# Kernel optimization log

Measured on AMD Instinct MI355X. Metric: run time of the kernel, lower is better.

The kernel has to match this reference:

```python
import jax, jax.numpy as jnp
import numpy as np

B, S, D, H = 4, 2048, 1024, 4
HD = D // H


def setup_inputs() -> dict:
    key = jax.random.key(0)
    ks = jax.random.split(key, 6)
    s = 0.02  # init scale for projection weights
    return {
        "hidden_states": jax.random.normal(ks[0], (B, S, D), jnp.float32),
        "Wq": jax.random.normal(ks[1], (D, D), jnp.float32) * s,
        "Wk": jax.random.normal(ks[2], (D, D), jnp.float32) * s,
        "Wv": jax.random.normal(ks[3], (D, D), jnp.float32) * s,
        "Wo": jax.random.normal(ks[4], (D, D), jnp.float32) * s,
        "bo": jnp.zeros((D,), jnp.float32),
        "betas": jax.random.normal(ks[5], (1, H, 1, 1), jnp.float32),
        "mem": jnp.zeros((H, HD, HD), jnp.float32),
        "z": jnp.zeros((H, HD, 1), jnp.float32),
    }


def reference(hidden_states, Wq, Wk, Wv, Wo, bo, betas, mem, z):
    b, s, d = hidden_states.shape
    h = betas.shape[1]
    hd = d // h

    def split(x):  # [b,s,d] -> [b,h,s,hd]
        return x.reshape(b, s, h, hd).transpose(0, 2, 1, 3)

    q = split(hidden_states @ Wq.T)
    k = split(hidden_states @ Wk.T)
    v = split(hidden_states @ Wv.T)

    # standard causal attention (note: no 1/sqrt(d) scaling, faithful to source)
    aw = jnp.einsum('bhqd,bhkd->bhqk', q, k)
    causal = jnp.tril(jnp.ones((s, s), bool))
    aw = jnp.where(causal, aw, jnp.finfo(aw.dtype).min)
    p = jax.nn.softmax(aw, axis=-1)
    attn = jnp.einsum('bhqk,bhkd->bhqd', p, v)

    # linear-attention memory read
    sq = jax.nn.elu(q) + 1.0
    sk = jax.nn.elu(k) + 1.0
    A_mem = jnp.einsum('bhsd,hde->bhse', sq, mem) / (
        jnp.einsum('bhsd,hdo->bhso', sq, z) + 1e-6)

    # sigmoid-gated blend
    g = jax.nn.sigmoid(betas)
    out = g * A_mem + (1.0 - g) * attn

    # memory / z state update (delta rule), averaged over batch
    delta = jnp.einsum('bhsd,hde->bhse', sk, mem) / (
        jnp.einsum('bhsd,hdo->bhso', sk, z) + 1e-6)
    mem_new = mem + jnp.einsum('bhsd,bhse->hde', sk, v - delta) / b
    z_new = z + jnp.mean(jnp.sum(sk, axis=2), axis=0)[:, :, None]

    # merge heads + output projection
    out = out.transpose(0, 2, 1, 3).reshape(b, s, d)
    out = out @ Wo.T + bo
    return (out, mem_new, z_new)
```

## Files before the change

kernel.cpp:

```cpp
#include <hip/hip_runtime.h>

#define Bsz 4
#define Ssz 2048
#define Dsz 1024
#define Hsz 4
#define HDsz 256
#define Msz 8192
#define LOG2E 1.4426950408889634f

typedef unsigned short u16;
typedef __attribute__((ext_vector_type(8))) short bf16x8;
typedef __attribute__((ext_vector_type(4))) float f32x4;

__device__ __forceinline__ u16 f2b(float f) {
  unsigned u = __float_as_uint(f);
  return (u16)((u + 0x7FFFu + ((u >> 16) & 1u)) >> 16);
}
__device__ __forceinline__ unsigned pk2(float a, float b) {
  return (unsigned)f2b(a) | ((unsigned)f2b(b) << 16);
}
__device__ __forceinline__ float ex2(float x) {
#if __has_builtin(__builtin_amdgcn_exp2f)
  return __builtin_amdgcn_exp2f(x);
#else
  return exp2f(x);
#endif
}

typedef const unsigned int __attribute__((address_space(1)))* gcp;
typedef unsigned int __attribute__((address_space(3)))* lcp;
__device__ __forceinline__ void gld16(const u16* g, u16* l) {
  __builtin_amdgcn_global_load_lds((gcp)g, (lcp)l, 16, 0, 0);
}

__global__ __launch_bounds__(256) void cvt_bf16(const float4* __restrict__ in,
                                                u16* __restrict__ outp) {
  size_t i = (size_t)blockIdx.x * 256 + threadIdx.x;
  float4 v = in[i];
  uint2 r; r.x = pk2(v.x, v.y); r.y = pk2(v.z, v.w);
  *(uint2*)(outp + i * 4) = r;
}

__global__ __launch_bounds__(256) void gemm_lds(const u16* __restrict__ A16,
                                                const u16* __restrict__ Wb,
                                                const float* __restrict__ bias,
                                                float* __restrict__ C32,
                                                u16* __restrict__ Cbf,
                                                float cbfs) {
  __shared__ u16 sA[128 * 64];
  __shared__ u16 sB[128 * 64];
  const int tid = threadIdx.x;
  const int lane = tid & 63, quad = lane >> 4, l15 = lane & 15;
  const int w = tid >> 6;
  const int mw = (w >> 1) * 64, nw = (w & 1) * 64;
  const int bid = blockIdx.y * 8 + blockIdx.x;
  const int nb = (bid & 7) * 64 + (bid >> 3);
  const int m0 = (nb >> 3) * 128, n0 = (nb & 7) * 128;
  const int r0 = tid >> 3;
  const int seg = ((tid & 7) ^ (r0 & 7)) * 8;
  const u16* ga0 = A16 + (size_t)(m0 + r0) * Dsz + seg;
  const u16* gb0 = Wb + (size_t)(n0 + r0) * Dsz + seg;
  f32x4 acc[4][4] = {};
  for (int k0 = 0; k0 < Dsz; k0 += 64) {
    __syncthreads();
#pragma unroll
    for (int i = 0; i < 4; ++i) {
      gld16(ga0 + (size_t)(i * 32) * Dsz + k0, sA + i * 2048 + w * 512);
      gld16(gb0 + (size_t)(i * 32) * Dsz + k0, sB + i * 2048 + w * 512);
    }
    __syncthreads();
#pragma unroll
    for (int dd = 0; dd < 2; ++dd) {
      bf16x8 af[4], bfr[4];
#pragma unroll
      for (int i = 0; i < 4; ++i) {
        const int sl = ((quad + 4 * dd) ^ (l15 & 7)) * 8;
        af[i] = *(const bf16x8*)&sA[(mw + i * 16 + l15) * 64 + sl];
        bfr[i] = *(const bf16x8*)&sB[(nw + i * 16 + l15) * 64 + sl];
      }
#pragma unroll
      for (int i = 0; i < 4; ++i)
#pragma unroll
        for (int j = 0; j < 4; ++j)
          acc[i][j] = __builtin_amdgcn_mfma_f32_16x16x32_bf16(af[i], bfr[j], acc[i][j], 0, 0, 0);
    }
  }
#pragma unroll
  for (int j = 0; j < 4; ++j) {
    const int n = n0 + nw + j * 16 + l15;
    const float bv = bias ? bias[n] : 0.f;
#pragma unroll
    for (int i = 0; i < 4; ++i) {
#pragma unroll
      for (int r = 0; r < 4; ++r) {
        const int m = m0 + mw + i * 16 + quad * 4 + r;
        const float val = acc[i][j][r] + bv;
        const size_t idx = (size_t)m * Dsz + n;
        if (C32) C32[idx] = val;
        if (Cbf) Cbf[idx] = f2b(val * cbfs);
      }
    }
  }
}

__global__ __launch_bounds__(256) void transpose_v(const float* __restrict__ V,
                                                   u16* __restrict__ Vt) {
  __shared__ u16 tile[32 * 36];
  const int t = threadIdx.x;
  const int s0 = blockIdx.x * 32, e0 = blockIdx.y * 32, bh = blockIdx.z;
  const int b = bh >> 2, h = bh & 3;
  {
    const int s_l = t >> 3, e8 = (t & 7) * 4;
    float4 v = *(const float4*)(V + ((size_t)(b * Ssz) + s0 + s_l) * Dsz + h * HDsz + e0 + e8);
    uint2 r; r.x = pk2(v.x, v.y); r.y = pk2(v.z, v.w);
    *(uint2*)&tile[s_l * 36 + e8] = r;
  }
  __syncthreads();
  {
    const int e_l = t >> 3, s4 = (t & 7) * 4;
    u16 a = tile[(s4 + 0) * 36 + e_l], b2 = tile[(s4 + 1) * 36 + e_l];
    u16 c = tile[(s4 + 2) * 36 + e_l], d = tile[(s4 + 3) * 36 + e_l];
    uint2 r; r.x = (unsigned)a | ((unsigned)b2 << 16);
    r.y = (unsigned)c | ((unsigned)d << 16);
    *(uint2*)(Vt + ((size_t)bh * HDsz + e0 + e_l) * Ssz + s0 + s4) = r;
  }
}

__global__ __launch_bounds__(256) void attn_mfma(const u16* __restrict__ Qg,
                                                 const u16* __restrict__ Kg,
                                                 const u16* __restrict__ Vtg,
                                                 float* __restrict__ At,
                                                 float* __restrict__ Pb,
                                                 float* __restrict__ mlb) {
  static const unsigned char tab[52] = {
      (unsigned char)(31|0x80), (unsigned char)(31|0xC0),
      (unsigned char)(30|0x80), (unsigned char)(30|0xC0),
      (unsigned char)(29|0x80), (unsigned char)(29|0xC0),
      (unsigned char)(28|0x80), (unsigned char)(28|0xC0),
      (unsigned char)(27|0x80), (unsigned char)(27|0xC0),
      (unsigned char)(26|0x80), (unsigned char)(26|0xC0),
      (unsigned char)(25|0x80), (unsigned char)(25|0xC0),
      (unsigned char)(24|0x80), (unsigned char)(24|0xC0),
      (unsigned char)(23|0x80), (unsigned char)(23|0xC0),
      11,
      (unsigned char)(22|0x80), (unsigned char)(22|0xC0),
      (unsigned char)(21|0x80), (unsigned char)(21|0xC0),
      10,
      (unsigned char)(20|0x80), (unsigned char)(20|0xC0),
      (unsigned char)(19|0x80), (unsigned char)(19|0xC0),
      9,
      (unsigned char)(18|0x80), (unsigned char)(18|0xC0),
      (unsigned char)(17|0x80), (unsigned char)(17|0xC0),
      8,
      (unsigned char)(16|0x80), (unsigned char)(16|0xC0),
      (unsigned char)(15|0x80), (unsigned char)(15|0xC0),
      7,
      (unsigned char)(14|0x80), (unsigned char)(14|0xC0),
      (unsigned char)(13|0x80), (unsigned char)(13|0xC0),
      6,
      (unsigned char)(12|0x80), (unsigned char)(12|0xC0),
      5, 4, 3, 2, 1, 0};
  const int e = tab[blockIdx.x];
  const int qt = e & 63, cc = (e >> 6) & 1;
  const bool split = (e >> 7) != 0;
  const int bh = blockIdx.y, b = bh >> 2, h = bh & 3;
  const int tid = threadIdx.x, w = tid >> 6, lane = tid & 63;
  const int quad = lane >> 4, l15 = lane & 15;
  __shared__ u16 sK[2][32 * 256];
  __shared__ u16 sV[256 * 32];
  const int q0w = qt * 64 + w * 16;
  bf16x8 qf[8];
  {
    const u16* qp = Qg + ((size_t)(b * Ssz) + q0w + l15) * Dsz + h * HDsz + quad * 8;
#pragma unroll
    for (int dd = 0; dd < 8; ++dd) qf[dd] = *(const bf16x8*)(qp + dd * 32);
  }
  f32x4 o[16] = {};
  float m_old = -1e30f, l = 0.f;
  const int nkt = 2 * qt + 2, half = qt + 1;
  const int kt_lo = (split && cc) ? half : 0;
  const int kt_hi = (split && !cc) ? half : nkt;
  const u16* kstage = Kg + ((size_t)(b * Ssz) + (tid >> 5)) * Dsz + h * HDsz
                      + (((tid & 31) ^ ((tid >> 5) & 7)) << 3);
  const u16* vstage = Vtg + ((size_t)bh * HDsz + (tid >> 2)) * Ssz
                      + (((tid & 3) ^ ((tid >> 3) & 3)) << 3);
  int bufc = 0;
  {
    const u16* kp = kstage + (size_t)(kt_lo * 32) * Dsz;
#pragma unroll
    for (int i = 0; i < 4; ++i)
      gld16(kp + (size_t)i * 8 * Dsz, &sK[0][w * 512 + i * 2048]);
  }
  for (int kt = kt_lo; kt < kt_hi; ++kt) {
    const int j0 = kt * 32;
    __syncthreads();
    {
      const u16* vp = vstage + kt * 32;
#pragma unroll
      for (int i = 0; i < 4; ++i)
        gld16(vp + (size_t)i * 64 * Ssz, &sV[w * 512 + i * 2048]);
    }
    if (kt + 1 < kt_hi) {
      const u16* kp = kstage + (size_t)((kt + 1) * 32) * Dsz;
      const int bn = bufc ^ 1;
#pragma unroll
      for (int i = 0; i < 4; ++i)
        gld16(kp + (size_t)i * 8 * Dsz, &sK[bn][w * 512 + i * 2048]);
    }
    f32x4 s0a = {}, s0b = {}, s1a = {}, s1b = {};
#pragma unroll
    for (int dd = 0; dd < 4; ++dd) {
      const int c0 = ((dd * 4 + quad) ^ (l15 & 7)) << 3;
      const int c1 = (((dd + 4) * 4 + quad) ^ (l15 & 7)) << 3;
      bf16x8 a0 = *(const bf16x8*)&sK[bufc][l15 * 256 + c0];
      bf16x8 a1 = *(const bf16x8*)&sK[bufc][(16 + l15) * 256 + c0];
      bf16x8 b0 = *(const bf16x8*)&sK[bufc][l15 * 256 + c1];
      bf16x8 b1 = *(const bf16x8*)&sK[bufc][(16 + l15) * 256 + c1];
      s0a = __builtin_amdgcn_mfma_f32_16x16x32_bf16(a0, qf[dd], s0a, 0, 0, 0);
      s1a = __builtin_amdgcn_mfma_f32_16x16x32_bf16(a1, qf[dd], s1a, 0, 0, 0);
      s0b = __builtin_amdgcn_mfma_f32_16x16x32_bf16(b0, qf[dd + 4], s0b, 0, 0, 0);
      s1b = __builtin_amdgcn_mfma_f32_16x16x32_bf16(b1, qf[dd + 4], s1b, 0, 0, 0);
    }
    f32x4 s0v = s0a + s0b, s1v = s1a + s1b;
    const int qg = q0w + l15;
    float p[8];
#pragma unroll
    for (int r = 0; r < 4; ++r) {
      const int kg = j0 + quad * 4 + r;
      p[r] = (kg <= qg) ? s0v[r] : -1e30f;
      p[4 + r] = (kg + 16 <= qg) ? s1v[r] : -1e30f;
    }
    float mt = fmaxf(fmaxf(fmaxf(p[0], p[1]), fmaxf(p[2], p[3])),
                     fmaxf(fmaxf(p[4], p[5]), fmaxf(p[6], p[7])));
    mt = fmaxf(mt, __shfl_xor(mt, 16));
    mt = fmaxf(mt, __shfl_xor(mt, 32));
    const bool keep = __all(mt - m_old <= 11.0f);
    const float m_new = keep ? m_old : fmaxf(m_old, mt);
    float ts = 0.f;
#pragma unroll
    for (int i = 0; i < 8; ++i) { p[i] = ex2(p[i] - m_new); ts += p[i]; }
    ts += __shfl_xor(ts, 16);
    ts += __shfl_xor(ts, 32);
    if (keep) {
      l += ts;
    } else {
      const float alpha = ex2(m_old - m_new);
      l = l * alpha + ts;
      m_old = m_new;
      const float a0_ = __shfl(alpha, (lane & 48) | (quad * 4 + 0));
      const float a1_ = __shfl(alpha, (lane & 48) | (quad * 4 + 1));
      const float a2_ = __shfl(alpha, (lane & 48) | (quad * 4 + 2));
      const float a3_ = __shfl(alpha, (lane & 48) | (quad * 4 + 3));
#pragma unroll
      for (int ds = 0; ds < 16; ++ds) {
        o[ds][0] *= a0_; o[ds][1] *= a1_; o[ds][2] *= a2_; o[ds][3] *= a3_;
      }
    }
    const unsigned a0p = pk2(p[0], p[1]), a1p = pk2(p[2], p[3]);
    const unsigned b0p = pk2(p[4], p[5]), b1p = pk2(p[6], p[7]);
    const int sAl = l15 | ((quad & 1) << 5);
    const int sBl = sAl | 16;
    const unsigned xa0 = __shfl(a0p, sAl), xa1 = __shfl(a1p, sAl);
    const unsigned xb0 = __shfl(b0p, sAl), xb1 = __shfl(b1p, sAl);
    const unsigned ya0 = __shfl(a0p, sBl), ya1 = __shfl(a1p, sBl);
    const unsigned yb0 = __shfl(b0p, sBl), yb1 = __shfl(b1p, sBl);
    const bool hi2 = quad >= 2;
    uint4 pkv;
    pkv.x = hi2 ? xb0 : xa0;
    pkv.y = hi2 ? xb1 : xa1;
    pkv.z = hi2 ? yb0 : ya0;
    pkv.w = hi2 ? yb1 : ya1;
    bf16x8 pf = *(bf16x8*)&pkv;
    const int vc0 = (quad ^ ((l15 >> 1) & 3)) << 3;
    __syncthreads();
#pragma unroll
    for (int ds = 0; ds < 16; ++ds) {
      bf16x8 bv = *(const bf16x8*)&sV[(ds * 16 + l15) * 32 + vc0];
      o[ds] = __builtin_amdgcn_mfma_f32_16x16x32_bf16(pf, bv, o[ds], 0, 0, 0);
    }
    bufc ^= 1;
  }
  if (!split) {
    float lr[4];
#pragma unroll
    for (int r = 0; r < 4; ++r) lr[r] = 1.f / __shfl(l, (lane & 48) | (quad * 4 + r));
    float* ob = At + ((size_t)bh * Ssz + q0w + quad * 4) * HDsz + l15;
#pragma unroll
    for (int r = 0; r < 4; ++r)
#pragma unroll
      for (int ds = 0; ds < 16; ++ds)
        ob[(size_t)r * HDsz + ds * 16] = o[ds][r] * lr[r];
  } else {
    float* dst;
    if (cc == 0)
      dst = At + ((size_t)bh * Ssz + q0w + quad * 4) * HDsz + l15;
    else
      dst = Pb + ((size_t)((bh * 20 + (qt - 12)) * 64) + w * 16 + quad * 4) * HDsz + l15;
#pragma unroll
    for (int r = 0; r < 4; ++r)
#pragma unroll
      for (int ds = 0; ds < 16; ++ds)
        dst[(size_t)r * HDsz + ds * 16] = o[ds][r];
    if (lane < 16) {
      const int idx = (bh * 20 + (qt - 12)) * 64 + w * 16 + l15;
      mlb[cc * 40960 + idx] = m_old;
      mlb[cc * 40960 + 20480 + idx] = l;
    }
  }
}

__global__ __launch_bounds__(256) void attn_merge(float* __restrict__ At,
                                                  const float* __restrict__ Pb,
                                                  const float* __restrict__ mlb) {
  const int qx = blockIdx.x, bh = blockIdx.y;
  const int t = threadIdx.x;
  const int slot = (bh * 20 + qx) * 64;
  float4* abase = (float4*)(At + ((size_t)bh * Ssz + (12 + qx) * 64) * HDsz);
  const float4* pbase = (const float4*)(Pb + (size_t)slot * HDsz);
#pragma unroll
  for (int i = 0; i < 16; ++i) {
    const int f = i * 256 + t;
    const int qr = f >> 6;
    const int idx = slot + qr;
    const float m0 = mlb[idx], l0 = mlb[20480 + idx];
    const float m1 = mlb[40960 + idx], l1 = mlb[61440 + idx];
    const float mm = fmaxf(m0, m1);
    const float w0 = ex2(m0 - mm), w1 = ex2(m1 - mm);
    const float inv = 1.f / (l0 * w0 + l1 * w1);
    float4 av = abase[f];
    float4 pv = pbase[f];
    float4 ov;
    ov.x = (av.x * w0 + pv.x * w1) * inv;
    ov.y = (av.y * w0 + pv.y * w1) * inv;
    ov.z = (av.z * w0 + pv.z * w1) * inv;
    ov.w = (av.w * w0 + pv.w * w1) * inv;
    abase[f] = ov;
  }
}

__global__ __launch_bounds__(256) void eludens(float* __restrict__ Qb,
                                               float* __restrict__ Kb,
                                               const float* __restrict__ z,
                                               float* __restrict__ dq,
                                               float* __restrict__ dk) {
  const int wid = threadIdx.x >> 6, lane = threadIdx.x & 63;
  const int r = blockIdx.x * 4 + wid;
  const int b = r >> 13, h = (r >> 11) & 3, s = r & 2047;
  const size_t base = ((size_t)(b * Ssz + s)) * Dsz + h * HDsz + lane * 4;
  float4 z4 = *(const float4*)(z + h * HDsz + lane * 4);
  float4 q = *(float4*)(Qb + base);
  q.x = q.x > 0.f ? q.x + 1.f : __expf(q.x);
  q.y = q.y > 0.f ? q.y + 1.f : __expf(q.y);
  q.z = q.z > 0.f ? q.z + 1.f : __expf(q.z);
  q.w = q.w > 0.f ? q.w + 1.f : __expf(q.w);
  *(float4*)(Qb + base) = q;
  float4 k = *(float4*)(Kb + base);
  k.x = k.x > 0.f ? k.x + 1.f : __expf(k.x);
  k.y = k.y > 0.f ? k.y + 1.f : __expf(k.y);
  k.z = k.z > 0.f ? k.z + 1.f : __expf(k.z);
  k.w = k.w > 0.f ? k.w + 1.f : __expf(k.w);
  *(float4*)(Kb + base) = k;
  float pq = q.x * z4.x + q.y * z4.y + q.z * z4.z + q.w * z4.w;
  float pk = k.x * z4.x + k.y * z4.y + k.z * z4.z + k.w * z4.w;
#pragma unroll
  for (int off = 32; off; off >>= 1) {
    pq += __shfl_down(pq, off);
    pk += __shfl_down(pk, off);
  }
  if (lane == 0) { dq[r] = pq; dk[r] = pk; }
}

__global__ __launch_bounds__(256) void memread_mfma(const float* __restrict__ Asrc,
                                                    const float* __restrict__ mem,
                                                    const float* __restrict__ dens,
                                                    const float* __restrict__ betas,
                                                    const float* __restrict__ At,
                                                    float* __restrict__ Vio,
                                                    u16* __restrict__ bfout, int mode) {
  const int h = blockIdx.z;
  const int tid = threadIdx.x, lane = tid & 63, w = tid >> 6;
  const int quad = lane >> 4, l15 = lane & 15;
  const int mw = (w >> 1) * 64, ew = (w & 1) * 64;
  const int m0 = blockIdx.y * 128, e0t = blockIdx.x * 128;
  __shared__ u16 sA[128 * 40];
  __shared__ u16 sB[128 * 40];
  const int srow = tid >> 1, sseg = (tid & 1) * 16;
  const int k4 = (tid & 7) * 4, e4 = (tid >> 3) * 4;
  f32x4 acc[4][4] = {};
  for (int k0 = 0; k0 < HDsz; k0 += 32) {
    __syncthreads();
    {
      const float* ap = Asrc + (size_t)(m0 + srow) * Dsz + h * HDsz + k0 + sseg;
      float4 f0 = *(const float4*)ap, f1 = *(const float4*)(ap + 4);
      float4 f2 = *(const float4*)(ap + 8), f3 = *(const float4*)(ap + 12);
      uint4 u0, u1;
      u0.x = pk2(f0.x, f0.y); u0.y = pk2(f0.z, f0.w);
      u0.z = pk2(f1.x, f1.y); u0.w = pk2(f1.z, f1.w);
      u1.x = pk2(f2.x, f2.y); u1.y = pk2(f2.z, f2.w);
      u1.z = pk2(f3.x, f3.y); u1.w = pk2(f3.z, f3.w);
      u16* dst = &sA[srow * 40 + sseg];
      *(uint4*)dst = u0; *(uint4*)(dst + 8) = u1;
    }
    {
      const float* bp = mem + (size_t)h * 65536 + (size_t)(k0 + k4) * HDsz + e0t + e4;
      float4 r0 = *(const float4*)bp;
      float4 r1 = *(const float4*)(bp + HDsz);
      float4 r2 = *(const float4*)(bp + 2 * HDsz);
      float4 r3 = *(const float4*)(bp + 3 * HDsz);
      const float* rr[4] = {(const float*)&r0, (const float*)&r1,
                            (const float*)&r2, (const float*)&r3};
#pragma unroll
      for (int c = 0; c < 4; ++c) {
        uint2 u;
        u.x = pk2(rr[0][c], rr[1][c]);
        u.y = pk2(rr[2][c], rr[3][c]);
        *(uint2*)&sB[(e4 + c) * 40 + k4] = u;
      }
    }
    __syncthreads();
    bf16x8 af[4], bfr[4];
#pragma unroll
    for (int i = 0; i < 4; ++i) {
      af[i] = *(const bf16x8*)&sA[(mw + i * 16 + l15) * 40 + quad * 8];
      bfr[i] = *(const bf16x8*)&sB[(ew + i * 16 + l15) * 40 + quad * 8];
    }
#pragma unroll
    for (int i = 0; i < 4; ++i)
#pragma unroll
      for (int j = 0; j < 4; ++j)
        acc[i][j] = __builtin_amdgcn_mfma_f32_16x16x32_bf16(af[i], bfr[j], acc[i][j], 0, 0, 0);
  }
  const float g = 1.f / (1.f + __expf(-betas[h]));
#pragma unroll
  for (int i = 0; i < 4; ++i) {
#pragma unroll
    for (int r = 0; r < 4; ++r) {
      const int m = m0 + mw + i * 16 + quad * 4 + r;
      const int b = m >> 11, s = m & 2047;
      const int rowidx = ((b << 2) + h) * Ssz + s;
      const float inv = 1.f / (dens[rowidx] + 1e-6f);
#pragma unroll
      for (int j = 0; j < 4; ++j) {
        const int e = e0t + ew + j * 16 + l15;
        const float av = acc[i][j][r] * inv;
        if (mode == 0) {
          const float a = At[(size_t)rowidx * HDsz + e];
          bfout[(size_t)m * Dsz + h * HDsz + e] = f2b(g * av + (1.f - g) * a);
        } else {
          float* p = Vio + (size_t)m * Dsz + h * HDsz + e;
          *p = *p - av;
        }
      }
    }
  }
}

__global__ __launch_bounds__(256) void mem_update_mfma(const float* __restrict__ SK,
                                                       const float* __restrict__ W,
                                                       float* __restrict__ P) {
  const int de = blockIdx.x;
  const int d0 = (de >> 1) * 128, e0 = (de & 1) * 128;
  const int h = blockIdx.y, chunk = blockIdx.z;
  const int m0 = chunk * 512;
  const int tid = threadIdx.x, lane = tid & 63, w = tid >> 6;
  const int quad = lane >> 4, l15 = lane & 15;
  const int dw = (w >> 1) * 64, ew = (w & 1) * 64;
  __shared__ u16 sA[128 * 40];
  __shared__ u16 sB[128 * 40];
  const int m4 = (tid & 7) * 4;
  const int c4 = (tid >> 3) * 4;
  f32x4 acc[4][4] = {};
  for (int mt = 0; mt < 512; mt += 32) {
    __syncthreads();
    const float* ka = SK + (size_t)(m0 + mt + m4) * Dsz + h * HDsz + d0 + c4;
    const float* wa = W + (size_t)(m0 + mt + m4) * Dsz + h * HDsz + e0 + c4;
    float4 a0 = *(const float4*)ka;
    float4 a1 = *(const float4*)(ka + Dsz);
    float4 a2 = *(const float4*)(ka + 2 * Dsz);
    float4 a3 = *(const float4*)(ka + 3 * Dsz);
    float4 b0 = *(const float4*)wa;
    float4 b1 = *(const float4*)(wa + Dsz);
    float4 b2 = *(const float4*)(wa + 2 * Dsz);
    float4 b3 = *(const float4*)(wa + 3 * Dsz);
    const float* aa[4] = {(const float*)&a0, (const float*)&a1,
                          (const float*)&a2, (const float*)&a3};
    const float* bb[4] = {(const float*)&b0, (const float*)&b1,
                          (const float*)&b2, (const float*)&b3};
#pragma unroll
    for (int c = 0; c < 4; ++c) {
      uint2 ua, ub2;
      ua.x = pk2(aa[0][c], aa[1][c]); ua.y = pk2(aa[2][c], aa[3][c]);
      ub2.x = pk2(bb[0][c], bb[1][c]); ub2.y = pk2(bb[2][c], bb[3][c]);
      *(uint2*)&sA[(c4 + c) * 40 + m4] = ua;
      *(uint2*)&sB[(c4 + c) * 40 + m4] = ub2;
    }
    __syncthreads();
    bf16x8 af[4], bfr[4];
#pragma unroll
    for (int i = 0; i < 4; ++i) {
      af[i] = *(const bf16x8*)&sA[(dw + i * 16 + l15) * 40 + quad * 8];
      bfr[i] = *(const bf16x8*)&sB[(ew + i * 16 + l15) * 40 + quad * 8];
    }
#pragma unroll
    for (int i = 0; i < 4; ++i)
#pragma unroll
      for (int j = 0; j < 4; ++j)
        acc[i][j] = __builtin_amdgcn_mfma_f32_16x16x32_bf16(af[i], bfr[j], acc[i][j], 0, 0, 0);
  }
  float* Pp = P + ((size_t)(h * 16 + chunk)) * 65536;
#pragma unroll
  for (int i = 0; i < 4; ++i)
#pragma unroll
    for (int r = 0; r < 4; ++r) {
      const int d = d0 + dw + i * 16 + quad * 4 + r;
#pragma unroll
      for (int j = 0; j < 4; ++j) {
        const int e = e0 + ew + j * 16 + l15;
        Pp[(size_t)d * HDsz + e] = acc[i][j][r];
      }
    }
}

__global__ __launch_bounds__(256) void mem_reduce(const float4* __restrict__ P,
                                                  const float4* __restrict__ mem,
                                                  float4* __restrict__ outmem) {
  const int gid = blockIdx.x * 256 + threadIdx.x;
  const int h = gid >> 14, off = gid & 16383;
  float sx = 0.f, sy = 0.f, sz = 0.f, sw = 0.f;
#pragma unroll 4
  for (int c = 0; c < 16; ++c) {
    float4 v = P[((size_t)(h * 16 + c) << 14) + off];
    sx += v.x; sy += v.y; sz += v.z; sw += v.w;
  }
  float4 m = mem[gid];
  float4 o;
  o.x = m.x + 0.25f * sx; o.y = m.y + 0.25f * sy;
  o.z = m.z + 0.25f * sz; o.w = m.w + 0.25f * sw;
  outmem[gid] = o;
}

__global__ __launch_bounds__(256) void z_update(const float* __restrict__ SK,
                                                const float* __restrict__ z_in,
                                                float* __restrict__ z_out) {
  __shared__ float4 red[256];
  const int h = blockIdx.x >> 7, chunk = blockIdx.x & 127;
  const int wid = threadIdx.x >> 6, lane = threadIdx.x & 63;
  const int m0 = chunk * 64;
  float4 s = {0.f, 0.f, 0.f, 0.f};
#pragma unroll
  for (int i = 0; i < 16; ++i) {
    const int row = m0 + i * 4 + wid;
    float4 v = *(const float4*)(SK + (size_t)row * Dsz + h * HDsz + lane * 4);
    s.x += v.x; s.y += v.y; s.z += v.z; s.w += v.w;
  }
  red[wid * 64 + lane] = s;
  __syncthreads();
  if (wid == 0) {
    float4 a = red[lane], b = red[64 + lane], c = red[128 + lane], d = red[192 + lane];
    a.x = (a.x + b.x + c.x + d.x) * 0.25f;
    a.y = (a.y + b.y + c.y + d.y) * 0.25f;
    a.z = (a.z + b.z + c.z + d.z) * 0.25f;
    a.w = (a.w + b.w + c.w + d.w) * 0.25f;
    if (chunk == 0) {
      const float4 z4 = *(const float4*)(z_in + h * HDsz + lane * 4);
      a.x += z4.x; a.y += z4.y; a.z += z4.z; a.w += z4.w;
    }
    float* zp = z_out + h * HDsz + lane * 4;
    atomicAdd(zp + 0, a.x);
    atomicAdd(zp + 1, a.y);
    atomicAdd(zp + 2, a.z);
    atomicAdd(zp + 3, a.w);
  }
}

extern "C" void kernel_launch(void* const* d_in, const int* in_sizes, int n_in,
                              void* d_out, int out_size, void* d_ws, size_t ws_size,
                              hipStream_t stream) {
  (void)in_sizes; (void)n_in; (void)out_size; (void)ws_size;
  const float* Hs = (const float*)d_in[0];
  const float* Wq = (const float*)d_in[1];
  const float* Wk = (const float*)d_in[2];
  const float* Wv = (const float*)d_in[3];
  const float* Wo = (const float*)d_in[4];
  const float* bo = (const float*)d_in[5];
  const float* betas = (const float*)d_in[6];
  const float* mem = (const float*)d_in[7];
  const float* z = (const float*)d_in[8];

  float* ws = (float*)d_ws;
  float* Qb = ws;
  float* Kb = ws + 8388608;
  float* Vb = ws + 16777216;
  float* At = ws + 25165824;
  float* dq = ws + 33554432;
  float* dk = ws + 33587200;
  float* mlb = ws + 33619968;
  u16* ub = (u16*)(ws + 33701888);
  u16* Wqb = ub;
  u16* Wkb = ub + 1048576;
  u16* Wvb = ub + 2097152;
  u16* Wob = ub + 3145728;
  u16* Qbf = ub + 4194304;
  u16* Kbf = ub + 12582912;
  u16* Vt = ub + 20971520;
  u16* Hsb = Vt;
  float* P = (float*)Vt;
  float* Pb = (float*)d_out;

  float* out = (float*)d_out;
  float* outmem = out + (size_t)Msz * Dsz;
  float* outz = outmem + Hsz * HDsz * HDsz;

  hipMemsetAsync(outz, 0, (size_t)(Hsz * HDsz) * sizeof(float), stream);

  cvt_bf16<<<1024, 256, 0, stream>>>((const float4*)Wq, Wqb);
  cvt_bf16<<<1024, 256, 0, stream>>>((const float4*)Wk, Wkb);
  cvt_bf16<<<1024, 256, 0, stream>>>((const float4*)Wv, Wvb);
  cvt_bf16<<<1024, 256, 0, stream>>>((const float4*)Wo, Wob);
  cvt_bf16<<<8192, 256, 0, stream>>>((const float4*)Hs, Hsb);

  dim3 gg(8, 64);
  gemm_lds<<<gg, 256, 0, stream>>>(Hsb, Wqb, nullptr, Qb, Qbf, LOG2E);
  gemm_lds<<<gg, 256, 0, stream>>>(Hsb, Wkb, nullptr, Kb, Kbf, 1.f);
  gemm_lds<<<gg, 256, 0, stream>>>(Hsb, Wvb, nullptr, Vb, nullptr, 1.f);

  transpose_v<<<dim3(64, 8, 16), 256, 0, stream>>>(Vb, Vt);
  attn_mfma<<<dim3(52, 16), 256, 0, stream>>>(Qbf, Kbf, Vt, At, Pb, mlb);
  attn_merge<<<dim3(20, 16), 256, 0, stream>>>(At, Pb, mlb);

  eludens<<<8192, 256, 0, stream>>>(Qb, Kb, z, dq, dk);

  memread_mfma<<<dim3(2, 64, 4), 256, 0, stream>>>(Qb, mem, dq, betas, At, nullptr, Qbf, 0);
  memread_mfma<<<dim3(2, 64, 4), 256, 0, stream>>>(Kb, mem, dk, betas, nullptr, Vb, nullptr, 1);

  mem_update_mfma<<<dim3(4, 4, 16), 256, 0, stream>>>(Kb, Vb, P);
  mem_reduce<<<256, 256, 0, stream>>>((const float4*)P, (const float4*)mem, (float4*)outmem);
  z_update<<<512, 256, 0, stream>>>(Kb, z, outz);

  gemm_lds<<<gg, 256, 0, stream>>>(Qbf, Wob, bo, out, nullptr, 1.f);
}
```

Measured before the change: 498.8 us.

## Precompute bf16 and transposed operands for memory read and update GEMMs

The elu activations are now written out as bf16 when they are computed, mem is transposed to bf16 once, and both sk and v-delta are pre-transposed into seq-major bf16 buffers. memread and mem_update then load swizzled 64-wide K tiles directly with gld16 instead of reading fp32, converting it and transposing it inside the GEMM loop. This aims to cut global traffic and in-loop conversion work. In exchange it adds three transpose kernels and reuses workspace buffers as aliases, which carries overwrite risk.

```diff
diff --git a/kernel.cpp b/kernel.cpp
--- a/kernel.cpp
+++ b/kernel.cpp
@@ -123,6 +123,50 @@
     uint2 r; r.x = (unsigned)a | ((unsigned)b2 << 16);
     r.y = (unsigned)c | ((unsigned)d << 16);
     *(uint2*)(Vt + ((size_t)bh * HDsz + e0 + e_l) * Ssz + s0 + s4) = r;
+  }
+}
+
+__global__ __launch_bounds__(256) void transpose_b16(const u16* __restrict__ src,
+                                                     u16* __restrict__ dst) {
+  __shared__ u16 tile[32 * 36];
+  const int t = threadIdx.x;
+  const int s0 = blockIdx.x * 32, c0 = blockIdx.y * 32, bh = blockIdx.z;
+  const int b = bh >> 2, h = bh & 3;
+  {
+    const int s_l = t >> 3, c8 = (t & 7) * 4;
+    uint2 v = *(const uint2*)(src + ((size_t)(b * Ssz) + s0 + s_l) * Dsz + h * HDsz + c0 + c8);
+    *(uint2*)&tile[s_l * 36 + c8] = v;
+  }
+  __syncthreads();
+  {
+    const int c_l = t >> 3, s4 = (t & 7) * 4;
+    u16 a = tile[(s4 + 0) * 36 + c_l], b2 = tile[(s4 + 1) * 36 + c_l];
+    u16 c = tile[(s4 + 2) * 36 + c_l], d = tile[(s4 + 3) * 36 + c_l];
+    uint2 r; r.x = (unsigned)a | ((unsigned)b2 << 16);
+    r.y = (unsigned)c | ((unsigned)d << 16);
+    *(uint2*)(dst + ((size_t)bh * HDsz + c0 + c_l) * Ssz + s0 + s4) = r;
+  }
+}
+
+__global__ __launch_bounds__(256) void transpose_mem(const float* __restrict__ mem,
+                                                     u16* __restrict__ memT) {
+  __shared__ u16 tile[32 * 36];
+  const int t = threadIdx.x;
+  const int d0 = blockIdx.x * 32, e0 = blockIdx.y * 32, h = blockIdx.z;
+  {
+    const int d_l = t >> 3, e8 = (t & 7) * 4;
+    float4 v = *(const float4*)(mem + (size_t)h * 65536 + (size_t)(d0 + d_l) * HDsz + e0 + e8);
+    uint2 r; r.x = pk2(v.x, v.y); r.y = pk2(v.z, v.w);
+    *(uint2*)&tile[d_l * 36 + e8] = r;
+  }
+  __syncthreads();
+  {
+    const int e_l = t >> 3, d4 = (t & 7) * 4;
+    u16 a = tile[(d4 + 0) * 36 + e_l], b2 = tile[(d4 + 1) * 36 + e_l];
+    u16 c = tile[(d4 + 2) * 36 + e_l], d = tile[(d4 + 3) * 36 + e_l];
+    uint2 r; r.x = (unsigned)a | ((unsigned)b2 << 16);
+    r.y = (unsigned)c | ((unsigned)d << 16);
+    *(uint2*)(memT + (size_t)h * 65536 + (size_t)(e0 + e_l) * HDsz + d0 + d4) = r;
   }
 }
 
@@ -342,7 +386,9 @@
                                                float* __restrict__ Kb,
                                                const float* __restrict__ z,
                                                float* __restrict__ dq,
-                                               float* __restrict__ dk) {
+                                               float* __restrict__ dk,
+                                               u16* __restrict__ SQb,
+                                               u16* __restrict__ SKb) {
   const int wid = threadIdx.x >> 6, lane = threadIdx.x & 63;
   const int r = blockIdx.x * 4 + wid;
   const int b = r >> 13, h = (r >> 11) & 3, s = r & 2047;
@@ -354,12 +400,16 @@
   q.z = q.z > 0.f ? q.z + 1.f : __expf(q.z);
   q.w = q.w > 0.f ? q.w + 1.f : __expf(q.w);
   *(float4*)(Qb + base) = q;
+  { uint2 qb; qb.x = pk2(q.x, q.y); qb.y = pk2(q.z, q.w);
+    *(uint2*)(SQb + base) = qb; }
   float4 k = *(float4*)(Kb + base);
   k.x = k.x > 0.f ? k.x + 1.f : __expf(k.x);
   k.y = k.y > 0.f ? k.y + 1.f : __expf(k.y);
   k.z = k.z > 0.f ? k.z + 1.f : __expf(k.z);
   k.w = k.w > 0.f ? k.w + 1.f : __expf(k.w);
   *(float4*)(Kb + base) = k;
+  { uint2 kb; kb.x = pk2(k.x, k.y); kb.y = pk2(k.z, k.w);
+    *(uint2*)(SKb + base) = kb; }
   float pq = q.x * z4.x + q.y * z4.y + q.z * z4.z + q.w * z4.w;
   float pk = k.x * z4.x + k.y * z4.y + k.z * z4.z + k.w * z4.w;
 #pragma unroll
@@ -370,65 +420,48 @@
   if (lane == 0) { dq[r] = pq; dk[r] = pk; }
 }
 
-__global__ __launch_bounds__(256) void memread_mfma(const float* __restrict__ Asrc,
-                                                    const float* __restrict__ mem,
+__global__ __launch_bounds__(256) void memread_mfma(const u16* __restrict__ A16,
+                                                    const u16* __restrict__ memT,
                                                     const float* __restrict__ dens,
                                                     const float* __restrict__ betas,
                                                     const float* __restrict__ At,
-                                                    float* __restrict__ Vio,
+                                                    const float* __restrict__ Vb,
                                                     u16* __restrict__ bfout, int mode) {
+  __shared__ u16 sA[128 * 64];
+  __shared__ u16 sB[128 * 64];
   const int h = blockIdx.z;
   const int tid = threadIdx.x, lane = tid & 63, w = tid >> 6;
   const int quad = lane >> 4, l15 = lane & 15;
   const int mw = (w >> 1) * 64, ew = (w & 1) * 64;
   const int m0 = blockIdx.y * 128, e0t = blockIdx.x * 128;
-  __shared__ u16 sA[128 * 40];
-  __shared__ u16 sB[128 * 40];
-  const int srow = tid >> 1, sseg = (tid & 1) * 16;
-  const int k4 = (tid & 7) * 4, e4 = (tid >> 3) * 4;
+  const int r0 = tid >> 3;
+  const int seg = ((tid & 7) ^ (r0 & 7)) * 8;
+  const u16* ga0 = A16 + (size_t)(m0 + r0) * Dsz + h * HDsz + seg;
+  const u16* gb0 = memT + (size_t)h * 65536 + (size_t)(e0t + r0) * HDsz + seg;
   f32x4 acc[4][4] = {};
-  for (int k0 = 0; k0 < HDsz; k0 += 32) {
-    __syncthreads();
-    {
-      const float* ap = Asrc + (size_t)(m0 + srow) * Dsz + h * HDsz + k0 + sseg;
-      float4 f0 = *(const float4*)ap, f1 = *(const float4*)(ap + 4);
-      float4 f2 = *(const float4*)(ap + 8), f3 = *(const float4*)(ap + 12);
-      uint4 u0, u1;
-      u0.x = pk2(f0.x, f0.y); u0.y = pk2(f0.z, f0.w);
-      u0.z = pk2(f1.x, f1.y); u0.w = pk2(f1.z, f1.w);
-      u1.x = pk2(f2.x, f2.y); u1.y = pk2(f2.z, f2.w);
-      u1.z = pk2(f3.x, f3.y); u1.w = pk2(f3.z, f3.w);
-      u16* dst = &sA[srow * 40 + sseg];
-      *(uint4*)dst = u0; *(uint4*)(dst + 8) = u1;
-    }
-    {
-      const float* bp = mem + (size_t)h * 65536 + (size_t)(k0 + k4) * HDsz + e0t + e4;
-      float4 r0 = *(const float4*)bp;
-      float4 r1 = *(const float4*)(bp + HDsz);
-      float4 r2 = *(const float4*)(bp + 2 * HDsz);
-      float4 r3 = *(const float4*)(bp + 3 * HDsz);
-      const float* rr[4] = {(const float*)&r0, (const float*)&r1,
-                            (const float*)&r2, (const float*)&r3};
-#pragma unroll
-      for (int c = 0; c < 4; ++c) {
-        uint2 u;
-        u.x = pk2(rr[0][c], rr[1][c]);
-        u.y = pk2(rr[2][c], rr[3][c]);
-        *(uint2*)&sB[(e4 + c) * 40 + k4] = u;
+  for (int k0 = 0; k0 < HDsz; k0 += 64) {
+    __syncthreads();
+#pragma unroll
+    for (int i = 0; i < 4; ++i) {
+      gld16(ga0 + (size_t)(i * 32) * Dsz + k0, sA + i * 2048 + w * 512);
+      gld16(gb0 + (size_t)(i * 32) * HDsz + k0, sB + i * 2048 + w * 512);
+    }
+    __syncthreads();
+#pragma unroll
+    for (int dd = 0; dd < 2; ++dd) {
+      bf16x8 af[4], bfr[4];
+#pragma unroll
+      for (int i = 0; i < 4; ++i) {
+        const int sl = ((quad + 4 * dd) ^ (l15 & 7)) * 8;
+        af[i] = *(const bf16x8*)&sA[(mw + i * 16 + l15) * 64 + sl];
+        bfr[i] = *(const bf16x8*)&sB[(ew + i * 16 + l15) * 64 + sl];
       }
-    }
-    __syncthreads();
-    bf16x8 af[4], bfr[4];
-#pragma unroll
-    for (int i = 0; i < 4; ++i) {
-      af[i] = *(const bf16x8*)&sA[(mw + i * 16 + l15) * 40 + quad * 8];
-      bfr[i] = *(const bf16x8*)&sB[(ew + i * 16 + l15) * 40 + quad * 8];
-    }
-#pragma unroll
-    for (int i = 0; i < 4; ++i)
-#pragma unroll
-      for (int j = 0; j < 4; ++j)
-        acc[i][j] = __builtin_amdgcn_mfma_f32_16x16x32_bf16(af[i], bfr[j], acc[i][j], 0, 0, 0);
+#pragma unroll
+      for (int i = 0; i < 4; ++i)
+#pragma unroll
+        for (int j = 0; j < 4; ++j)
+          acc[i][j] = __builtin_amdgcn_mfma_f32_16x16x32_bf16(af[i], bfr[j], acc[i][j], 0, 0, 0);
+    }
   }
   const float g = 1.f / (1.f + __expf(-betas[h]));
 #pragma unroll
@@ -447,65 +480,55 @@
           const float a = At[(size_t)rowidx * HDsz + e];
           bfout[(size_t)m * Dsz + h * HDsz + e] = f2b(g * av + (1.f - g) * a);
         } else {
-          float* p = Vio + (size_t)m * Dsz + h * HDsz + e;
-          *p = *p - av;
+          const float vv = Vb[(size_t)m * Dsz + h * HDsz + e];
+          bfout[(size_t)m * Dsz + h * HDsz + e] = f2b(vv - av);
         }
       }
     }
   }
 }
 
-__global__ __launch_bounds__(256) void mem_update_mfma(const float* __restrict__ SK,
-                                                       const float* __restrict__ W,
+__global__ __launch_bounds__(256) void mem_update_mfma(const u16* __restrict__ SKt,
+                                                       const u16* __restrict__ Wt,
                                                        float* __restrict__ P) {
+  __shared__ u16 sA[128 * 64];
+  __shared__ u16 sB[128 * 64];
   const int de = blockIdx.x;
   const int d0 = (de >> 1) * 128, e0 = (de & 1) * 128;
   const int h = blockIdx.y, chunk = blockIdx.z;
-  const int m0 = chunk * 512;
+  const int b = chunk >> 2, s0 = (chunk & 3) * 512;
+  const int bh = b * 4 + h;
   const int tid = threadIdx.x, lane = tid & 63, w = tid >> 6;
   const int quad = lane >> 4, l15 = lane & 15;
   const int dw = (w >> 1) * 64, ew = (w & 1) * 64;
-  __shared__ u16 sA[128 * 40];
-  __shared__ u16 sB[128 * 40];
-  const int m4 = (tid & 7) * 4;
-  const int c4 = (tid >> 3) * 4;
+  const int r0 = tid >> 3;
+  const int seg = ((tid & 7) ^ (r0 & 7)) * 8;
+  const u16* ga0 = SKt + ((size_t)bh * HDsz + d0 + r0) * Ssz + s0 + seg;
+  const u16* gb0 = Wt + ((size_t)bh * HDsz + e0 + r0) * Ssz + s0 + seg;
   f32x4 acc[4][4] = {};
-  for (int mt = 0; mt < 512; mt += 32) {
-    __syncthreads();
-    const float* ka = SK + (size_t)(m0 + mt + m4) * Dsz + h * HDsz + d0 + c4;
-    const float* wa = W + (size_t)(m0 + mt + m4) * Dsz + h * HDsz + e0 + c4;
-    float4 a0 = *(const float4*)ka;
-    float4 a1 = *(const float4*)(ka + Dsz);
-    float4 a2 = *(const float4*)(ka + 2 * Dsz);
-    float4 a3 = *(const float4*)(ka + 3 * Dsz);
-    float4 b0 = *(const float4*)wa;
-    float4 b1 = *(const float4*)(wa + Dsz);
-    float4 b2 = *(const float4*)(wa + 2 * Dsz);
-    float4 b3 = *(const float4*)(wa + 3 * Dsz);
-    const float* aa[4] = {(const float*)&a0, (const float*)&a1,
-                          (const float*)&a2, (const float*)&a3};
-    const float* bb[4] = {(const float*)&b0, (const float*)&b1,
-                          (const float*)&b2, (const float*)&b3};
-#pragma unroll
-    for (int c = 0; c < 4; ++c) {
-      uint2 ua, ub2;
-      ua.x = pk2(aa[0][c], aa[1][c]); ua.y = pk2(aa[2][c], aa[3][c]);
-      ub2.x = pk2(bb[0][c], bb[1][c]); ub2.y = pk2(bb[2][c], bb[3][c]);
-      *(uint2*)&sA[(c4 + c) * 40 + m4] = ua;
-      *(uint2*)&sB[(c4 + c) * 40 + m4] = ub2;
-    }
-    __syncthreads();
-    bf16x8 af[4], bfr[4];
+  for (int kk = 0; kk < 512; kk += 64) {
+    __syncthreads();
 #pragma unroll
     for (int i = 0; i < 4; ++i) {
-      af[i] = *(const bf16x8*)&sA[(dw + i * 16 + l15) * 40 + quad * 8];
-      bfr[i] = *(const bf16x8*)&sB[(ew + i * 16 + l15) * 40 + quad * 8];
-    }
-#pragma unroll
-    for (int i = 0; i < 4; ++i)
-#pragma unroll
-      for (int j = 0; j < 4; ++j)
-        acc[i][j] = __builtin_amdgcn_mfma_f32_16x16x32_bf16(af[i], bfr[j], acc[i][j], 0, 0, 0);
+      gld16(ga0 + (size_t)(i * 32) * Ssz + kk, sA + i * 2048 + w * 512);
+      gld16(gb0 + (size_t)(i * 32) * Ssz + kk, sB + i * 2048 + w * 512);
+    }
+    __syncthreads();
+#pragma unroll
+    for (int dd = 0; dd < 2; ++dd) {
+      bf16x8 af[4], bfr[4];
+#pragma unroll
+      for (int i = 0; i < 4; ++i) {
+        const int sl = ((quad + 4 * dd) ^ (l15 & 7)) * 8;
+        af[i] = *(const bf16x8*)&sA[(dw + i * 16 + l15) * 64 + sl];
+        bfr[i] = *(const bf16x8*)&sB[(ew + i * 16 + l15) * 64 + sl];
+      }
+#pragma unroll
+      for (int i = 0; i < 4; ++i)
+#pragma unroll
+        for (int j = 0; j < 4; ++j)
+          acc[i][j] = __builtin_amdgcn_mfma_f32_16x16x32_bf16(af[i], bfr[j], acc[i][j], 0, 0, 0);
+    }
   }
   float* Pp = P + ((size_t)(h * 16 + chunk)) * 65536;
 #pragma unroll
@@ -604,8 +627,14 @@
   u16* Kbf = ub + 12582912;
   u16* Vt = ub + 20971520;
   u16* Hsb = Vt;
-  float* P = (float*)Vt;
+  u16* SQb = ub + 29360128;
+  u16* memT = ub + 37748736;
+  u16* SKb = Kbf;
+  u16* SKt = Vt;
+  u16* Wb16 = (u16*)At;
+  u16* Wt = (u16*)Qb;
   float* Pb = (float*)d_out;
+  float* P = (float*)d_out;
 
   float* out = (float*)d_out;
   float* outmem = out + (size_t)Msz * Dsz;
@@ -618,6 +647,7 @@
   cvt_bf16<<<1024, 256, 0, stream>>>((const float4*)Wv, Wvb);
   cvt_bf16<<<1024, 256, 0, stream>>>((const float4*)Wo, Wob);
   cvt_bf16<<<8192, 256, 0, stream>>>((const float4*)Hs, Hsb);
+  transpose_mem<<<dim3(8, 8, 4), 256, 0, stream>>>(mem, memT);
 
   dim3 gg(8, 64);
   gemm_lds<<<gg, 256, 0, stream>>>(Hsb, Wqb, nullptr, Qb, Qbf, LOG2E);
@@ -628,12 +658,14 @@
   attn_mfma<<<dim3(52, 16), 256, 0, stream>>>(Qbf, Kbf, Vt, At, Pb, mlb);
   attn_merge<<<dim3(20, 16), 256, 0, stream>>>(At, Pb, mlb);
 
-  eludens<<<8192, 256, 0, stream>>>(Qb, Kb, z, dq, dk);
-
-  memread_mfma<<<dim3(2, 64, 4), 256, 0, stream>>>(Qb, mem, dq, betas, At, nullptr, Qbf, 0);
-  memread_mfma<<<dim3(2, 64, 4), 256, 0, stream>>>(Kb, mem, dk, betas, nullptr, Vb, nullptr, 1);
-
-  mem_update_mfma<<<dim3(4, 4, 16), 256, 0, stream>>>(Kb, Vb, P);
+  eludens<<<8192, 256, 0, stream>>>(Qb, Kb, z, dq, dk, SQb, SKb);
+  transpose_b16<<<dim3(64, 8, 16), 256, 0, stream>>>(SKb, SKt);
+
+  memread_mfma<<<dim3(2, 64, 4), 256, 0, stream>>>(SQb, memT, dq, betas, At, nullptr, Qbf, 0);
+  memread_mfma<<<dim3(2, 64, 4), 256, 0, stream>>>(SKb, memT, dk, betas, nullptr, Vb, Wb16, 1);
+  transpose_b16<<<dim3(64, 8, 16), 256, 0, stream>>>(Wb16, Wt);
+
+  mem_update_mfma<<<dim3(4, 4, 16), 256, 0, stream>>>(SKt, Wt, P);
   mem_reduce<<<256, 256, 0, stream>>>((const float4*)P, (const float4*)mem, (float4*)outmem);
   z_update<<<512, 256, 0, stream>>>(Kb, z, outz);
 
```

After: 487.1 us. 1.02x faster.
